# Performance work log

Measured on AMD Instinct MI355X. Metric: run time of the kernel, lower is better.

Reference implementation:

```python
import jax, jax.numpy as jnp
import numpy as np


def setup_inputs() -> dict:
    key = jax.random.key(0)
    k1, k2 = jax.random.split(key)
    B, N, LENGTH = 2048, 64, 8
    # x: (batch, 2, n, n) -- real/imag planes of batched complex matrices
    x = jax.random.normal(k1, (B, 2, N, N), dtype=jnp.float32) * 0.1
    # learned coefficients: (length, 2, n, n), scaled down like the factorial-decaying init
    coefficients = jax.random.normal(k2, (LENGTH, 2, N, N), dtype=jnp.float32) * 0.05
    return {"x": x, "coefficients": coefficients}


def reference(x, coefficients):
    # Faithful port of MatrixMPowerSeriesLayer.call (including the sign used
    # for res_imag inside the i>=2 loop, which differs from the i==1 term).
    length = coefficients.shape[0]
    n = x.shape[2]
    xr = x[:, 0]  # (b, n, n)
    xi = x[:, 1]
    cr = coefficients[:, 0]  # (length, n, n)
    ci = coefficients[:, 1]
    unit = jnp.eye(n, dtype=x.dtype)

    tr, ti = xr, xi  # running complex power x^p
    # order-0 term: unit @ c[0] (broadcasts against batched terms)
    res_r = unit @ cr[0] + (jnp.einsum('bjk,kl->bjl', tr, cr[1]) - jnp.einsum('bjk,kl->bjl', ti, ci[1]))
    res_i = unit @ ci[0] + (jnp.einsum('bjk,kl->bjl', tr, ci[1]) + jnp.einsum('bjk,kl->bjl', ti, cr[1]))

    for i in range(2, length):
        # complex batched matmul: tmp <- tmp @ x
        new_tr = jnp.einsum('bjk,bkl->bjl', tr, xr) - jnp.einsum('bjk,bkl->bjl', ti, xi)
        ti = jnp.einsum('bjk,bkl->bjl', tr, xi) + jnp.einsum('bjk,bkl->bjl', ti, xr)
        tr = new_tr
        res_r = res_r + jnp.einsum('bjk,kl->bjl', tr, cr[i]) - jnp.einsum('bjk,kl->bjl', ti, ci[i])
        # NOTE: original code subtracts ti @ cr[i] here (not adds) -- kept faithful.
        res_i = res_i + jnp.einsum('bjk,kl->bjl', tr, ci[i]) - jnp.einsum('bjk,kl->bjl', ti, cr[i])

    return jnp.stack([res_r, res_i], axis=1)  # (b, 2, n, n)
```

## Files before the change

### kernel.cpp

```cpp
#include <hip/hip_runtime.h>

typedef __attribute__((ext_vector_type(4))) short short4v;
typedef __attribute__((ext_vector_type(8))) short short8v;
typedef __attribute__((ext_vector_type(2))) unsigned int uint2v;
typedef __attribute__((ext_vector_type(4))) unsigned int uint4v;
typedef __attribute__((ext_vector_type(4))) float f32x4;
typedef __attribute__((ext_vector_type(16))) float f32x16;

#define LSTRIDE 68
#define MATB (64 * LSTRIDE * 2)
#define REGA 0
#define REGB (4 * MATB)
#define LDS_BYTES (8 * MATB)

#define CFRAG_BYTES (7 * 4 * 2 * 4 * 1024)
#define INIT_OFF CFRAG_BYTES

__device__ __forceinline__ short bf16h(float v) {
    union { float f; unsigned u; } x; x.f = v;
    unsigned r = x.u + 0x7FFFu + ((x.u >> 16) & 1u);
    return (short)(r >> 16);
}
__device__ __forceinline__ float bf16tof(short s) {
    union { unsigned u; float f; } x; x.u = ((unsigned)(unsigned short)s) << 16;
    return x.f;
}
struct HL { unsigned h, l; };
__device__ __forceinline__ HL split2(float v0, float v1) {
    unsigned hp, lp;
    asm("v_cvt_pk_bf16_f32 %0, %1, %2" : "=v"(hp) : "v"(v0), "v"(v1));
    union { unsigned u; float f; } a, b;
    a.u = hp << 16;
    b.u = hp & 0xffff0000u;
    float l0 = v0 - a.f, l1 = v1 - b.f;
    asm("v_cvt_pk_bf16_f32 %0, %1, %2" : "=v"(lp) : "v"(l0), "v"(l1));
    HL r; r.h = hp; r.l = lp; return r;
}
__device__ __forceinline__ f32x16 MF(short8v a, short8v b, f32x16 c) {
    return __builtin_amdgcn_mfma_f32_32x32x16_bf16(a, b, c, 0, 0, 0);
}
__device__ __forceinline__ short8v negf(short8v a) {
    uint4v u = __builtin_bit_cast(uint4v, a);
    u ^= 0x80008000u;
    return __builtin_bit_cast(short8v, u);
}

__global__ void pms_prep(const float* __restrict__ coef, char* __restrict__ wsb) {
    const int blk = blockIdx.x;
    const int lane = threadIdx.x;
    const int lrow = lane & 31, lhi = lane >> 5;
    if (blk < 56) {
        const int qr  = blk & 1;
        const int km  = blk >> 1;
        const int mat = km & 3;
        const int kk  = km >> 2;
        const int part = mat >> 1;
        const int lo   = mat & 1;
        const float* C = coef + (size_t)((kk + 1) * 2 + part) * 4096;
        for (int t = 0; t < 4; ++t) {
            short8v o;
            #pragma unroll
            for (int j = 0; j < 8; ++j) {
                int krow = 16 * t + 8 * lhi + j;
                int col  = 32 * qr + lrow;
                float v = C[krow * 64 + col];
                short hh = bf16h(v);
                o[j] = lo ? bf16h(v - bf16tof(hh)) : hh;
            }
            *(short8v*)(wsb + ((size_t)blk * 4 + t) * 1024 + lane * 16) = o;
        }
    } else {
        const int id = blk - 56;
        const int qc = id & 1, qr = (id >> 1) & 1, part = id >> 2;
        const float* C0 = coef + (size_t)part * 4096;
        float* dst = (float*)(wsb + INIT_OFF + (size_t)(((part * 2 + qr) * 2 + qc) * 64 + lane) * 64);
        #pragma unroll
        for (int v = 0; v < 16; ++v) {
            int r = 32 * qr + (v & 3) + 8 * (v >> 2) + 4 * lhi;
            int c = 32 * qc + lrow;
            dst[v] = C0[c * 64 + r];
        }
    }
}

__global__ __launch_bounds__(256, 2) void pms_main(
    const float* __restrict__ x, const char* __restrict__ wsb,
    float* __restrict__ out)
{
    extern __shared__ char smem[];
    const int tid  = threadIdx.x;
    const int lane = tid & 63;
    const int w    = tid >> 6;
    const int qr = w >> 1, qc = w & 1;
    const int lrow = lane & 31, lhi = lane >> 5;
    const size_t b = blockIdx.x;
    const float* xb = x + b * 8192;

    #pragma unroll
    for (int s = 0; s < 8; ++s) {
        int f = s * 1024 + tid * 4;
        int p = f >> 12, m = (f >> 6) & 63, c = f & 63;
        f32x4 v = *(const f32x4*)(xb + f);
        HL a01 = split2(v[0], v[1]);
        HL a23 = split2(v[2], v[3]);
        uint2v h, l;
        h[0] = a01.h; l[0] = a01.l;
        h[1] = a23.h; l[1] = a23.l;
        int off = (m * LSTRIDE + c) * 2;
        *(uint2v*)(smem + REGA + (p * 2 + 0) * MATB + off) = h;
        *(uint2v*)(smem + REGA + (p * 2 + 1) * MATB + off) = l;
    }
    __syncthreads();

    short8v xa[2][2][4];
    #pragma unroll
    for (int pi = 0; pi < 2; ++pi)
    #pragma unroll
    for (int hl = 0; hl < 2; ++hl)
    #pragma unroll
    for (int t = 0; t < 4; ++t) {
        const short* mp = (const short*)(smem + REGA + (pi * 2 + hl) * MATB);
        short8v a;
        #pragma unroll
        for (int j = 0; j < 8; ++j)
            a[j] = mp[(16 * t + 8 * lhi + j) * LSTRIDE + 32 * qr + lrow];
        xa[pi][hl][t] = a;
    }

    f32x16 accRr, accRi;
    {
        const f32x4* p0 = (const f32x4*)(wsb + INIT_OFF + (size_t)(((0 + qr) * 2 + qc) * 64 + lane) * 64);
        const f32x4* p1 = (const f32x4*)(wsb + INIT_OFF + (size_t)(((2 + qr) * 2 + qc) * 64 + lane) * 64);
        #pragma unroll
        for (int g = 0; g < 4; ++g) {
            f32x4 a = p0[g], c4 = p1[g];
            #pragma unroll
            for (int j = 0; j < 4; ++j) { accRr[4 * g + j] = a[j]; accRi[4 * g + j] = c4[j]; }
        }
    }

    auto ldB = [&](int rbase, int mat, int t) -> short8v {
        const short4v* p = (const short4v*)(smem + rbase + mat * MATB
                             + (32 * qc + lrow) * (LSTRIDE * 2) + 32 * t + 16 * lhi);
        short4v a = p[0], c4 = p[1];
        short8v r;
        #pragma unroll
        for (int j = 0; j < 4; ++j) { r[j] = a[j]; r[j + 4] = c4[j]; }
        return r;
    };

    int cur = REGA, nxt = REGB;

    for (int k = 2; k <= 7; ++k) {
        const char* cw = wsb + (size_t)(k - 2) * 32768;
        const bool k1 = (k == 2);

        short8v cRh[4], cRl[4], cIh[4], cIl[4];
        #pragma unroll
        for (int t = 0; t < 4; ++t) {
            cRh[t] = *(const short8v*)(cw + ((0 * 2 + qr) * 4 + t) * 1024 + lane * 16);
            cRl[t] = *(const short8v*)(cw + ((1 * 2 + qr) * 4 + t) * 1024 + lane * 16);
            cIh[t] = *(const short8v*)(cw + ((2 * 2 + qr) * 4 + t) * 1024 + lane * 16);
            cIl[t] = *(const short8v*)(cw + ((3 * 2 + qr) * 4 + t) * 1024 + lane * 16);
        }
        short8v Brh = ldB(cur, 0, 0), Brl = ldB(cur, 1, 0);
        short8v Bih = ldB(cur, 2, 0), Bil = ldB(cur, 3, 0);

        f32x16 aTr, aTi;
        #pragma unroll
        for (int v = 0; v < 16; ++v) { aTr[v] = 0.f; aTi[v] = 0.f; }

        #pragma unroll
        for (int t = 0; t < 4; ++t) {
            short8v Nrh, Nrl, Nih, Nil;
            if (t < 3) {
                Nrh = ldB(cur, 0, t + 1); Nrl = ldB(cur, 1, t + 1);
                Nih = ldB(cur, 2, t + 1); Nil = ldB(cur, 3, t + 1);
            }
            short8v nBih = negf(Bih), nBil = negf(Bil);
            short8v sBih = k1 ? Bih : nBih;
            short8v sBil = k1 ? Bil : nBil;

            __builtin_amdgcn_s_setprio(1);
            accRr = MF(cRh[t], Brh, accRr);
            accRi = MF(cIh[t], Brh, accRi);
            aTr   = MF(xa[0][0][t], Brh, aTr);
            aTi   = MF(xa[1][0][t], Brh, aTi);

            accRr = MF(cRh[t], Brl, accRr);
            accRi = MF(cIh[t], Brl, accRi);
            aTr   = MF(xa[0][0][t], Brl, aTr);
            aTi   = MF(xa[1][0][t], Brl, aTi);

            accRr = MF(cRl[t], Brh, accRr);
            accRi = MF(cIl[t], Brh, accRi);
            aTr   = MF(xa[0][1][t], Brh, aTr);
            aTi   = MF(xa[1][1][t], Brh, aTi);

            accRr = MF(cIh[t], nBih, accRr);
            accRi = MF(cRh[t], sBih, accRi);
            aTr   = MF(xa[1][0][t], nBih, aTr);
            aTi   = MF(xa[0][0][t], Bih, aTi);

            accRr = MF(cIh[t], nBil, accRr);
            accRi = MF(cRh[t], sBil, accRi);
            aTr   = MF(xa[1][0][t], nBil, aTr);
            aTi   = MF(xa[0][0][t], Bil, aTi);

            accRr = MF(cIl[t], nBih, accRr);
            accRi = MF(cRl[t], sBih, accRi);
            aTr   = MF(xa[1][1][t], nBih, aTr);
            aTi   = MF(xa[0][1][t], Bih, aTi);
            __builtin_amdgcn_s_setprio(0);

            if (t < 3) { Brh = Nrh; Brl = Nrl; Bih = Nih; Bil = Nil; }
        }

        {
            const int c = 32 * qc + lrow;
            #pragma unroll
            for (int g = 0; g < 4; ++g) {
                int rbse = 32 * qr + 8 * g + 4 * lhi;
                HL r01 = split2(aTr[4 * g + 0], aTr[4 * g + 1]);
                HL r23 = split2(aTr[4 * g + 2], aTr[4 * g + 3]);
                HL i01 = split2(aTi[4 * g + 0], aTi[4 * g + 1]);
                HL i23 = split2(aTi[4 * g + 2], aTi[4 * g + 3]);
                uint2v hr, lr, hi2, li2;
                hr[0] = r01.h; lr[0] = r01.l; hr[1] = r23.h; lr[1] = r23.l;
                hi2[0] = i01.h; li2[0] = i01.l; hi2[1] = i23.h; li2[1] = i23.l;
                int off = (c * LSTRIDE + rbse) * 2;
                *(uint2v*)(smem + nxt + 0 * MATB + off) = hr;
                *(uint2v*)(smem + nxt + 1 * MATB + off) = lr;
                *(uint2v*)(smem + nxt + 2 * MATB + off) = hi2;
                *(uint2v*)(smem + nxt + 3 * MATB + off) = li2;
            }
        }
        __syncthreads();
        int tmp = cur; cur = nxt; nxt = tmp;
    }

    {
        const char* cw = wsb + (size_t)6 * 32768;
        short8v cRh[4], cRl[4], cIh[4], cIl[4];
        #pragma unroll
        for (int t = 0; t < 4; ++t) {
            cRh[t] = *(const short8v*)(cw + ((0 * 2 + qr) * 4 + t) * 1024 + lane * 16);
            cRl[t] = *(const short8v*)(cw + ((1 * 2 + qr) * 4 + t) * 1024 + lane * 16);
            cIh[t] = *(const short8v*)(cw + ((2 * 2 + qr) * 4 + t) * 1024 + lane * 16);
            cIl[t] = *(const short8v*)(cw + ((3 * 2 + qr) * 4 + t) * 1024 + lane * 16);
        }
        short8v Brh = ldB(cur, 0, 0), Brl = ldB(cur, 1, 0);
        short8v Bih = ldB(cur, 2, 0), Bil = ldB(cur, 3, 0);
        #pragma unroll
        for (int t = 0; t < 4; ++t) {
            short8v Nrh, Nrl, Nih, Nil;
            if (t < 3) {
                Nrh = ldB(cur, 0, t + 1); Nrl = ldB(cur, 1, t + 1);
                Nih = ldB(cur, 2, t + 1); Nil = ldB(cur, 3, t + 1);
            }
            short8v nBih = negf(Bih), nBil = negf(Bil);

            __builtin_amdgcn_s_setprio(1);
            accRr = MF(cRh[t], Brh, accRr);
            accRi = MF(cIh[t], Brh, accRi);
            accRr = MF(cRh[t], Brl, accRr);
            accRi = MF(cIh[t], Brl, accRi);
            accRr = MF(cRl[t], Brh, accRr);
            accRi = MF(cIl[t], Brh, accRi);
            accRr = MF(cIh[t], nBih, accRr);
            accRi = MF(cRh[t], nBih, accRi);
            accRr = MF(cIh[t], nBil, accRr);
            accRi = MF(cRh[t], nBil, accRi);
            accRr = MF(cIl[t], nBih, accRr);
            accRi = MF(cRl[t], nBih, accRi);
            __builtin_amdgcn_s_setprio(0);

            if (t < 3) { Brh = Nrh; Brl = Nrl; Bih = Nih; Bil = Nil; }
        }
    }

    __syncthreads();
    {
        const int c = 32 * qc + lrow;
        #pragma unroll
        for (int g = 0; g < 4; ++g) {
            int rbse = 32 * qr + 8 * g + 4 * lhi;
            f32x4 vr, vi;
            #pragma unroll
            for (int j = 0; j < 4; ++j) { vr[j] = accRr[4 * g + j]; vi[j] = accRi[4 * g + j]; }
            *(f32x4*)(smem + nxt + (size_t)(0 * 4352 + c * LSTRIDE + rbse) * 4) = vr;
            *(f32x4*)(smem + nxt + (size_t)(1 * 4352 + c * LSTRIDE + rbse) * 4) = vi;
        }
    }
    __syncthreads();
    float* ob = out + b * 8192;
    #pragma unroll
    for (int s = 0; s < 8; ++s) {
        int f = s * 1024 + tid * 4;
        int p = f >> 12, m = (f >> 6) & 63, n = f & 63;
        *(f32x4*)(ob + f) = *(const f32x4*)(smem + nxt + (size_t)(p * 4352 + m * LSTRIDE + n) * 4);
    }
}

extern "C" void kernel_launch(void* const* d_in, const int* in_sizes, int n_in,
                              void* d_out, int out_size, void* d_ws, size_t ws_size,
                              hipStream_t stream) {
    const float* x    = (const float*)d_in[0];
    const float* coef = (const float*)d_in[1];
    float* out = (float*)d_out;
    char*  wsb = (char*)d_ws;
    const int B = in_sizes[0] / 8192;

    (void)hipFuncSetAttribute(reinterpret_cast<const void*>(&pms_main),
                              hipFuncAttributeMaxDynamicSharedMemorySize, LDS_BYTES);

    pms_prep<<<64, 64, 0, stream>>>(coef, wsb);
    pms_main<<<B, 256, LDS_BYTES, stream>>>(x, wsb, out);
}
```

Baseline: 144.4 us.

## Use Karatsuba-style 3-multiply complex products with Horner evaluation and smaller LDS

Adds a new kernel path that runs the power series in a Horner-like form, folding coefficient products into the running matrix. Each complex matmul uses three real products (Karatsuba/Gauss trick) with precomputed sum and difference planes in place of four. LDS drops from eight to six bf16 split planes, with launch bounds targeting two blocks per CU. The aim is fewer MFMA operations and higher occupancy, at the cost of extra add/split work, extra precomputed coefficient buffers, and possible precision changes from the bf16 hi/lo splitting of sums. The new path is taken only when the workspace is large enough, otherwise the old kernels run.

```diff
diff --git a/kernel.cpp b/kernel.cpp
--- a/kernel.cpp
+++ b/kernel.cpp
@@ -9,12 +9,18 @@
 
 #define LSTRIDE 68
 #define MATB (64 * LSTRIDE * 2)
+
 #define REGA 0
 #define REGB (4 * MATB)
 #define LDS_BYTES (8 * MATB)
-
 #define CFRAG_BYTES (7 * 4 * 2 * 4 * 1024)
 #define INIT_OFF CFRAG_BYTES
+
+#define KLDS (6 * MATB)
+#define KSLOT_STRIDE 49152
+#define CS_OFF (7 * KSLOT_STRIDE)
+#define KINIT_OFF (CS_OFF + 2 * 8192)
+#define KWS_NEED (KINIT_OFF + 32768)
 
 __device__ __forceinline__ short bf16h(float v) {
     union { float f; unsigned u; } x; x.f = v;
@@ -44,6 +50,318 @@
     u ^= 0x80008000u;
     return __builtin_bit_cast(short8v, u);
 }
+
+
+__global__ void pms_prep_k(const float* __restrict__ coef, char* __restrict__ wsb) {
+    const int blk = blockIdx.x;
+    const int lane = threadIdx.x;
+    const int lrow = lane & 31, lhi = lane >> 5;
+    if (blk < 84) {
+        const int s = blk / 12, rem = blk % 12;
+        const int mat = rem >> 1, qr = rem & 1;
+        const int which = mat >> 1, lo = mat & 1;
+        const float* Pr = coef + (size_t)((s + 1) * 2 + 0) * 4096;
+        const float* Pi = coef + (size_t)((s + 1) * 2 + 1) * 4096;
+        for (int t = 0; t < 4; ++t) {
+            short8v o;
+            #pragma unroll
+            for (int j = 0; j < 8; ++j) {
+                int idx = (16 * t + 8 * lhi + j) * 64 + 32 * qr + lrow;
+                float v = (which == 0) ? Pr[idx] : (which == 1) ? Pi[idx] : (Pi[idx] - Pr[idx]);
+                short hh = bf16h(v);
+                o[j] = lo ? bf16h(v - bf16tof(hh)) : hh;
+            }
+            *(short8v*)(wsb + (size_t)s * KSLOT_STRIDE + mat * 8192 + qr * 4096 + t * 1024 + lane * 16) = o;
+        }
+    } else if (blk < 88) {
+        const int id = blk - 84;
+        const int lo = id >> 1, qr = id & 1;
+        const float* Pr = coef + (size_t)(1 * 2 + 0) * 4096;
+        const float* Pi = coef + (size_t)(1 * 2 + 1) * 4096;
+        for (int t = 0; t < 4; ++t) {
+            short8v o;
+            #pragma unroll
+            for (int j = 0; j < 8; ++j) {
+                int idx = (16 * t + 8 * lhi + j) * 64 + 32 * qr + lrow;
+                float v = Pr[idx] + Pi[idx];
+                short hh = bf16h(v);
+                o[j] = lo ? bf16h(v - bf16tof(hh)) : hh;
+            }
+            *(short8v*)(wsb + CS_OFF + lo * 8192 + qr * 4096 + t * 1024 + lane * 16) = o;
+        }
+    } else {
+        const int id = blk - 88;
+        const int qc = id & 1, qr = (id >> 1) & 1, slot = id >> 2;
+        float* dst = (float*)(wsb + KINIT_OFF + (size_t)(((slot * 2 + qr) * 2 + qc) * 64 + lane) * 64);
+        #pragma unroll
+        for (int v = 0; v < 16; ++v) {
+            int r = 32 * qr + (v & 3) + 8 * (v >> 2) + 4 * lhi;
+            int c = 32 * qc + lrow;
+            float c0r = coef[c * 64 + r];
+            float c0i = coef[4096 + c * 64 + r];
+            dst[v] = (slot == 0) ? c0r : (c0i - c0r);
+        }
+    }
+}
+
+__global__ __launch_bounds__(256, 2) void pms_main_k(
+    const float* __restrict__ x, const char* __restrict__ wsb,
+    float* __restrict__ out)
+{
+    extern __shared__ char smem[];
+    const int tid  = threadIdx.x;
+    const int lane = tid & 63;
+    const int w    = tid >> 6;
+    const int qr = w >> 1, qc = w & 1;
+    const int lrow = lane & 31, lhi = lane >> 5;
+    const size_t b = blockIdx.x;
+    const float* xb = x + b * 8192;
+
+    #pragma unroll
+    for (int s = 0; s < 4; ++s) {
+        int f = s * 1024 + tid * 4;
+        int m = f >> 6, c = f & 63;
+        f32x4 vr = *(const f32x4*)(xb + f);
+        f32x4 vi = *(const f32x4*)(xb + 4096 + f);
+        f32x4 vs;
+        #pragma unroll
+        for (int j = 0; j < 4; ++j) vs[j] = vr[j] + vi[j];
+        HL r01 = split2(vr[0], vr[1]), r23 = split2(vr[2], vr[3]);
+        HL i01 = split2(vi[0], vi[1]), i23 = split2(vi[2], vi[3]);
+        HL s01 = split2(vs[0], vs[1]), s23 = split2(vs[2], vs[3]);
+        int off = (m * LSTRIDE + c) * 2;
+        uint2v u;
+        u[0] = r01.h; u[1] = r23.h; *(uint2v*)(smem + 0 * MATB + off) = u;
+        u[0] = r01.l; u[1] = r23.l; *(uint2v*)(smem + 1 * MATB + off) = u;
+        u[0] = i01.h; u[1] = i23.h; *(uint2v*)(smem + 2 * MATB + off) = u;
+        u[0] = i01.l; u[1] = i23.l; *(uint2v*)(smem + 3 * MATB + off) = u;
+        u[0] = s01.h; u[1] = s23.h; *(uint2v*)(smem + 4 * MATB + off) = u;
+        u[0] = s01.l; u[1] = s23.l; *(uint2v*)(smem + 5 * MATB + off) = u;
+    }
+    __syncthreads();
+
+    short8v xa[3][2][4];
+    #pragma unroll
+    for (int pi = 0; pi < 3; ++pi)
+    #pragma unroll
+    for (int hl = 0; hl < 2; ++hl)
+    #pragma unroll
+    for (int t = 0; t < 4; ++t) {
+        const short* mp = (const short*)(smem + (pi * 2 + hl) * MATB);
+        short8v a;
+        #pragma unroll
+        for (int j = 0; j < 8; ++j)
+            a[j] = mp[(16 * t + 8 * lhi + j) * LSTRIDE + 32 * qr + lrow];
+        xa[pi][hl][t] = a;
+    }
+
+    f32x16 accRr, accQ;
+    {
+        const f32x4* p0 = (const f32x4*)(wsb + KINIT_OFF + (size_t)(((0 + qr) * 2 + qc) * 64 + lane) * 64);
+        #pragma unroll
+        for (int g = 0; g < 4; ++g) {
+            f32x4 a = p0[g];
+            #pragma unroll
+            for (int j = 0; j < 4; ++j) { accRr[4 * g + j] = a[j]; accQ[4 * g + j] = 0.f; }
+        }
+    }
+
+    auto ldB = [&](int mat, int t) -> short8v {
+        const short4v* p = (const short4v*)(smem + mat * MATB
+                             + (32 * qc + lrow) * (LSTRIDE * 2) + 32 * t + 16 * lhi);
+        short4v a = p[0], c4 = p[1];
+        short8v r;
+        #pragma unroll
+        for (int j = 0; j < 4; ++j) { r[j] = a[j]; r[j + 4] = c4[j]; }
+        return r;
+    };
+
+    f32x16 m1, m2, m3;
+
+    auto foldWrite = [&]() {
+        const int c = 32 * qc + lrow;
+        f32x16 aTr, aTi, aTs;
+        #pragma unroll
+        for (int j = 0; j < 16; ++j) {
+            float ar = m1[j] - m2[j];
+            float ai = m3[j] - m1[j] - m2[j];
+            aTr[j] = ar; aTi[j] = ai; aTs[j] = ar + ai;
+        }
+        #pragma unroll
+        for (int g = 0; g < 4; ++g) {
+            int rbse = 32 * qr + 8 * g + 4 * lhi;
+            int off = (c * LSTRIDE + rbse) * 2;
+            HL a01 = split2(aTr[4 * g + 0], aTr[4 * g + 1]);
+            HL a23 = split2(aTr[4 * g + 2], aTr[4 * g + 3]);
+            HL b01 = split2(aTi[4 * g + 0], aTi[4 * g + 1]);
+            HL b23 = split2(aTi[4 * g + 2], aTi[4 * g + 3]);
+            HL c01 = split2(aTs[4 * g + 0], aTs[4 * g + 1]);
+            HL c23 = split2(aTs[4 * g + 2], aTs[4 * g + 3]);
+            uint2v u;
+            u[0] = a01.h; u[1] = a23.h; *(uint2v*)(smem + 0 * MATB + off) = u;
+            u[0] = a01.l; u[1] = a23.l; *(uint2v*)(smem + 1 * MATB + off) = u;
+            u[0] = b01.h; u[1] = b23.h; *(uint2v*)(smem + 2 * MATB + off) = u;
+            u[0] = b01.l; u[1] = b23.l; *(uint2v*)(smem + 3 * MATB + off) = u;
+            u[0] = c01.h; u[1] = c23.h; *(uint2v*)(smem + 4 * MATB + off) = u;
+            u[0] = c01.l; u[1] = c23.l; *(uint2v*)(smem + 5 * MATB + off) = u;
+        }
+    };
+
+    {
+        const char* cw = wsb;
+        #pragma unroll
+        for (int j = 0; j < 16; ++j) { m1[j] = 0.f; m2[j] = 0.f; m3[j] = 0.f; }
+        #pragma unroll
+        for (int t = 0; t < 4; ++t) {
+            short8v Crh = *(const short8v*)(cw + ((0 * 2 + qr) * 4 + t) * 1024 + lane * 16);
+            short8v Crl = *(const short8v*)(cw + ((1 * 2 + qr) * 4 + t) * 1024 + lane * 16);
+            short8v nCih = negf(*(const short8v*)(cw + ((2 * 2 + qr) * 4 + t) * 1024 + lane * 16));
+            short8v nCil = negf(*(const short8v*)(cw + ((3 * 2 + qr) * 4 + t) * 1024 + lane * 16));
+            short8v Cdh = *(const short8v*)(cw + ((4 * 2 + qr) * 4 + t) * 1024 + lane * 16);
+            short8v Cdl = *(const short8v*)(cw + ((5 * 2 + qr) * 4 + t) * 1024 + lane * 16);
+            short8v Csh = *(const short8v*)(wsb + CS_OFF + ((0 * 2 + qr) * 4 + t) * 1024 + lane * 16);
+            short8v Csl = *(const short8v*)(wsb + CS_OFF + ((1 * 2 + qr) * 4 + t) * 1024 + lane * 16);
+            short8v Brh = ldB(0, t), Brl = ldB(1, t);
+            short8v Bih = ldB(2, t), Bil = ldB(3, t);
+            short8v Bsh = ldB(4, t), Bsl = ldB(5, t);
+
+            __builtin_amdgcn_s_setprio(1);
+            accRr = MF(Crh, Brh, accRr);
+            accQ  = MF(Cdh, Brh, accQ);
+            m1    = MF(xa[0][0][t], Brh, m1);
+            accRr = MF(nCih, Bih, accRr);
+            accQ  = MF(Csh, Bih, accQ);
+            m2    = MF(xa[1][0][t], Bih, m2);
+            m3    = MF(xa[2][0][t], Bsh, m3);
+
+            accRr = MF(Crh, Brl, accRr);
+            accQ  = MF(Cdh, Brl, accQ);
+            m1    = MF(xa[0][0][t], Brl, m1);
+            accRr = MF(nCih, Bil, accRr);
+            accQ  = MF(Csh, Bil, accQ);
+            m2    = MF(xa[1][0][t], Bil, m2);
+            m3    = MF(xa[2][0][t], Bsl, m3);
+
+            accRr = MF(Crl, Brh, accRr);
+            accQ  = MF(Cdl, Brh, accQ);
+            m1    = MF(xa[0][1][t], Brh, m1);
+            accRr = MF(nCil, Bih, accRr);
+            accQ  = MF(Csl, Bih, accQ);
+            m2    = MF(xa[1][1][t], Bih, m2);
+            m3    = MF(xa[2][1][t], Bsh, m3);
+            __builtin_amdgcn_s_setprio(0);
+        }
+        __syncthreads();
+        foldWrite();
+        __syncthreads();
+    }
+
+    for (int ks = 1; ks <= 5; ++ks) {
+        const char* cw = wsb + (size_t)ks * KSLOT_STRIDE;
+        #pragma unroll
+        for (int j = 0; j < 16; ++j) { m1[j] = 0.f; m2[j] = 0.f; m3[j] = 0.f; }
+        #pragma unroll
+        for (int t = 0; t < 4; ++t) {
+            short8v Crh = *(const short8v*)(cw + ((0 * 2 + qr) * 4 + t) * 1024 + lane * 16);
+            short8v Crl = *(const short8v*)(cw + ((1 * 2 + qr) * 4 + t) * 1024 + lane * 16);
+            short8v nCih = negf(*(const short8v*)(cw + ((2 * 2 + qr) * 4 + t) * 1024 + lane * 16));
+            short8v nCil = negf(*(const short8v*)(cw + ((3 * 2 + qr) * 4 + t) * 1024 + lane * 16));
+            short8v Cdh = *(const short8v*)(cw + ((4 * 2 + qr) * 4 + t) * 1024 + lane * 16);
+            short8v Cdl = *(const short8v*)(cw + ((5 * 2 + qr) * 4 + t) * 1024 + lane * 16);
+            short8v Brh = ldB(0, t), Brl = ldB(1, t);
+            short8v Bih = ldB(2, t), Bil = ldB(3, t);
+            short8v Bsh = ldB(4, t), Bsl = ldB(5, t);
+
+            __builtin_amdgcn_s_setprio(1);
+            accRr = MF(Crh, Brh, accRr);
+            m1    = MF(xa[0][0][t], Brh, m1);
+            accQ  = MF(Cdh, Bsh, accQ);
+            accRr = MF(nCih, Bih, accRr);
+            m2    = MF(xa[1][0][t], Bih, m2);
+            m3    = MF(xa[2][0][t], Bsh, m3);
+
+            accRr = MF(Crh, Brl, accRr);
+            m1    = MF(xa[0][0][t], Brl, m1);
+            accQ  = MF(Cdh, Bsl, accQ);
+            accRr = MF(nCih, Bil, accRr);
+            m2    = MF(xa[1][0][t], Bil, m2);
+            m3    = MF(xa[2][0][t], Bsl, m3);
+
+            accRr = MF(Crl, Brh, accRr);
+            m1    = MF(xa[0][1][t], Brh, m1);
+            accQ  = MF(Cdl, Bsh, accQ);
+            accRr = MF(nCil, Bih, accRr);
+            m2    = MF(xa[1][1][t], Bih, m2);
+            m3    = MF(xa[2][1][t], Bsh, m3);
+            __builtin_amdgcn_s_setprio(0);
+        }
+        __syncthreads();
+        foldWrite();
+        __syncthreads();
+    }
+
+    {
+        const char* cw = wsb + (size_t)6 * KSLOT_STRIDE;
+        #pragma unroll
+        for (int t = 0; t < 4; ++t) {
+            short8v Crh = *(const short8v*)(cw + ((0 * 2 + qr) * 4 + t) * 1024 + lane * 16);
+            short8v Crl = *(const short8v*)(cw + ((1 * 2 + qr) * 4 + t) * 1024 + lane * 16);
+            short8v nCih = negf(*(const short8v*)(cw + ((2 * 2 + qr) * 4 + t) * 1024 + lane * 16));
+            short8v nCil = negf(*(const short8v*)(cw + ((3 * 2 + qr) * 4 + t) * 1024 + lane * 16));
+            short8v Cdh = *(const short8v*)(cw + ((4 * 2 + qr) * 4 + t) * 1024 + lane * 16);
+            short8v Cdl = *(const short8v*)(cw + ((5 * 2 + qr) * 4 + t) * 1024 + lane * 16);
+            short8v Brh = ldB(0, t), Brl = ldB(1, t);
+            short8v Bih = ldB(2, t), Bil = ldB(3, t);
+            short8v Bsh = ldB(4, t), Bsl = ldB(5, t);
+
+            __builtin_amdgcn_s_setprio(1);
+            accRr = MF(Crh, Brh, accRr);
+            accQ  = MF(Cdh, Bsh, accQ);
+            accRr = MF(nCih, Bih, accRr);
+            accRr = MF(Crh, Brl, accRr);
+            accQ  = MF(Cdh, Bsl, accQ);
+            accRr = MF(nCih, Bil, accRr);
+            accRr = MF(Crl, Brh, accRr);
+            accQ  = MF(Cdl, Bsh, accQ);
+            accRr = MF(nCil, Bih, accRr);
+            __builtin_amdgcn_s_setprio(0);
+        }
+    }
+
+    f32x16 accRi;
+    {
+        const f32x4* p1 = (const f32x4*)(wsb + KINIT_OFF + (size_t)(((2 + qr) * 2 + qc) * 64 + lane) * 64);
+        #pragma unroll
+        for (int g = 0; g < 4; ++g) {
+            f32x4 d = p1[g];
+            #pragma unroll
+            for (int j = 0; j < 4; ++j)
+                accRi[4 * g + j] = accRr[4 * g + j] + accQ[4 * g + j] + d[j];
+        }
+    }
+    __syncthreads();
+    {
+        const int c = 32 * qc + lrow;
+        #pragma unroll
+        for (int g = 0; g < 4; ++g) {
+            int rbse = 32 * qr + 8 * g + 4 * lhi;
+            f32x4 vr, vi;
+            #pragma unroll
+            for (int j = 0; j < 4; ++j) { vr[j] = accRr[4 * g + j]; vi[j] = accRi[4 * g + j]; }
+            *(f32x4*)(smem + (size_t)(0 * 4352 + c * LSTRIDE + rbse) * 4) = vr;
+            *(f32x4*)(smem + (size_t)(1 * 4352 + c * LSTRIDE + rbse) * 4) = vi;
+        }
+    }
+    __syncthreads();
+    float* ob = out + b * 8192;
+    #pragma unroll
+    for (int s = 0; s < 8; ++s) {
+        int f = s * 1024 + tid * 4;
+        int p = f >> 12, m = (f >> 6) & 63, n = f & 63;
+        *(f32x4*)(ob + f) = *(const f32x4*)(smem + (size_t)(p * 4352 + m * LSTRIDE + n) * 4);
+    }
+}
+
 
 __global__ void pms_prep(const float* __restrict__ coef, char* __restrict__ wsb) {
     const int blk = blockIdx.x;
@@ -311,9 +629,13 @@
     char*  wsb = (char*)d_ws;
     const int B = in_sizes[0] / 8192;
 
-    (void)hipFuncSetAttribute(reinterpret_cast<const void*>(&pms_main),
-                              hipFuncAttributeMaxDynamicSharedMemorySize, LDS_BYTES);
-
-    pms_prep<<<64, 64, 0, stream>>>(coef, wsb);
-    pms_main<<<B, 256, LDS_BYTES, stream>>>(x, wsb, out);
-}
+    if (ws_size >= (size_t)KWS_NEED) {
+        pms_prep_k<<<96, 64, 0, stream>>>(coef, wsb);
+        pms_main_k<<<B, 256, KLDS, stream>>>(x, wsb, out);
+    } else {
+        (void)hipFuncSetAttribute(reinterpret_cast<const void*>(&pms_main),
+                                  hipFuncAttributeMaxDynamicSharedMemorySize, LDS_BYTES);
+        pms_prep<<<64, 64, 0, stream>>>(coef, wsb);
+        pms_main<<<B, 256, LDS_BYTES, stream>>>(x, wsb, out);
+    }
+}
```

Result: slower. 205.3 us (+42.2%).
